# Optimization experiments

Measured on AMD Instinct MI355X. Metric: run time of the kernel, lower is better.

The kernel has to match this reference:

```python
import jax, jax.numpy as jnp
import numpy as np

N = 100000   # nodes
E = 3200000  # edges
C = 256      # in_channels
H = 64       # hidden_channels
G = 512      # graphs in batch
FC = [128, 64, 32, 16]
OUT = 2
EPS = 1e-5


def _linear(key, fan_in, fan_out):
    k1, k2 = jax.random.split(key)
    s = 1.0 / np.sqrt(fan_in)
    W = jax.random.uniform(k1, (fan_in, fan_out), jnp.float32, -s, s)
    b = jax.random.uniform(k2, (fan_out,), jnp.float32, -s, s)
    return W, b


def setup_inputs() -> dict:
    key = jax.random.key(0)
    ks = jax.random.split(key, 12)
    x = jax.random.normal(ks[0], (N, C), jnp.float32)
    edge_index = jax.random.randint(ks[1], (2, E), 0, N, dtype=jnp.int64)
    batch = jnp.sort(jax.random.randint(ks[2], (N,), 0, G, dtype=jnp.int64))
    w1, b1 = _linear(ks[3], C, H)
    w2, b2 = _linear(ks[4], H, H)
    g1 = jnp.ones((H,), jnp.float32); be1 = jnp.zeros((H,), jnp.float32)
    g2 = jnp.ones((H,), jnp.float32); be2 = jnp.zeros((H,), jnp.float32)
    fw1, fb1 = _linear(ks[5], H, FC[0])
    fw2, fb2 = _linear(ks[6], FC[0], FC[1])
    fw3, fb3 = _linear(ks[7], FC[1], FC[2])
    fw4, fb4 = _linear(ks[8], FC[2], FC[3])
    ow, ob = _linear(ks[9], FC[3], OUT)
    return dict(x=x, edge_index=edge_index, batch=batch,
                w1=w1, b1=b1, w2=w2, b2=b2,
                g1=g1, be1=be1, g2=g2, be2=be2,
                fw1=fw1, fb1=fb1, fw2=fw2, fb2=fb2,
                fw3=fw3, fb3=fb3, fw4=fw4, fb4=fb4,
                ow=ow, ob=ob)


def _gcn_layers(x, edge_index, w1, b1, w2, b2, g1, be1, g2, be2):
    # PyG GCNConv: add self loops, symmetric deg^-1/2 normalization, scatter-add at dst
    loops = jnp.arange(N, dtype=edge_index.dtype)
    src = jnp.concatenate([edge_index[0], loops])
    dst = jnp.concatenate([edge_index[1], loops])
    deg = jax.ops.segment_sum(jnp.ones((E + N,), jnp.float32), dst, num_segments=N)
    dis = jnp.where(deg > 0, jax.lax.rsqrt(jnp.maximum(deg, 1.0)), 0.0)
    norm = (dis[src] * dis[dst])[:, None]  # [E+N, 1]

    def conv(h, W, b):
        h = h @ W
        return jax.ops.segment_sum(h[src] * norm, dst, num_segments=N) + b

    def bn(h, g, be):  # BatchNorm1d over node dim (training-mode batch stats)
        m = jnp.mean(h, axis=0)
        v = jnp.var(h, axis=0)
        return (h - m) * jax.lax.rsqrt(v + EPS) * g + be

    h = bn(jax.nn.relu(conv(x, w1, b1)), g1, be1)   # dropout = identity (eval)
    h = bn(jax.nn.relu(conv(h, w2, b2)), g2, be2)
    return h


def reference(x, edge_index, batch, w1, b1, w2, b2, g1, be1, g2, be2,
              fw1, fb1, fw2, fb2, fw3, fb3, fw4, fb4, ow, ob):
    h = _gcn_layers(x, edge_index, w1, b1, w2, b2, g1, be1, g2, be2)
    # global_mean_pool over batch vector
    s = jax.ops.segment_sum(h, batch, num_segments=G)
    cnt = jax.ops.segment_sum(jnp.ones((N,), jnp.float32), batch, num_segments=G)
    p = s / jnp.maximum(cnt, 1.0)[:, None]  # [G, H]
    h = jax.nn.relu(p @ fw1 + fb1)
    h = jax.nn.relu(h @ fw2 + fb2)
    h = jax.nn.relu(h @ fw3 + fb3)
    h = jax.nn.relu(h @ fw4 + fb4)
    return h @ ow + ob  # [G, OUT]
```

## Files before the change

kernel.cpp:

```cpp
#include <hip/hip_runtime.h>
#include <hip/hip_fp16.h>

#define N_NODES 100000
#define E_EDGES 3200000
#define NG      512
#define BN_EPS  1e-5f

#define BSH     7
#define BNODES  128
#define NBUCK   782
#define NCHUNK  1024
#define CHUNK   3125

__global__ __launch_bounds__(256) void k_zero(float* __restrict__ stats1,
                                              float* __restrict__ stats2,
                                              float* __restrict__ sums,
                                              float* __restrict__ cnt) {
  int i = blockIdx.x * 256 + threadIdx.x;
  if (i < 128) { stats1[i] = 0.f; stats2[i] = 0.f; }
  if (i < NG * 64) sums[i] = 0.f;
  if (i < NG) cnt[i] = 0.f;
}

__global__ __launch_bounds__(256) void kb_hist(const int* __restrict__ ei,
                                               int* __restrict__ counts) {
  __shared__ int h[NBUCK];
  const int c = blockIdx.x, tid = threadIdx.x;
  for (int b = tid; b < NBUCK; b += 256) h[b] = 0;
  __syncthreads();
  const int* dst = ei + E_EDGES + c * CHUNK;
  for (int i = tid; i < CHUNK; i += 256) atomicAdd(&h[dst[i] >> BSH], 1);
  __syncthreads();
  for (int b = tid; b < NBUCK; b += 256) counts[b * NCHUNK + c] = h[b];
}

__global__ __launch_bounds__(1024) void kb_scan1(int* __restrict__ counts,
                                                 int* __restrict__ btot) {
  __shared__ int sm[NCHUNK];
  const int b = blockIdx.x, tid = threadIdx.x;
  const int cval = counts[b * NCHUNK + tid];
  int val = cval;
  sm[tid] = val;
  __syncthreads();
  for (int off = 1; off < NCHUNK; off <<= 1) {
    int t = (tid >= off) ? sm[tid - off] : 0;
    __syncthreads();
    val += t;
    sm[tid] = val;
    __syncthreads();
  }
  counts[b * NCHUNK + tid] = val - cval;
  if (tid == NCHUNK - 1) btot[b] = val;
}

__global__ __launch_bounds__(1024) void kb_scan2(const int* __restrict__ btot,
                                                 int* __restrict__ bbase) {
  __shared__ int sm[1024];
  const int tid = threadIdx.x;
  const int cval = (tid < NBUCK) ? btot[tid] : 0;
  int val = cval;
  sm[tid] = val;
  __syncthreads();
  for (int off = 1; off < 1024; off <<= 1) {
    int t = (tid >= off) ? sm[tid - off] : 0;
    __syncthreads();
    val += t;
    sm[tid] = val;
    __syncthreads();
  }
  if (tid < NBUCK) bbase[tid] = val - cval;
  if (tid == NBUCK - 1) bbase[NBUCK] = val;
}

__global__ __launch_bounds__(256) void kb_scatter(const int* __restrict__ ei,
                                                  const int* __restrict__ counts,
                                                  const int* __restrict__ bbase,
                                                  int* __restrict__ binned) {
  __shared__ int cur[NBUCK];
  const int c = blockIdx.x, tid = threadIdx.x;
  for (int b = tid; b < NBUCK; b += 256) cur[b] = bbase[b] + counts[b * NCHUNK + c];
  __syncthreads();
  const int* srcp = ei + c * CHUNK;
  const int* dstp = ei + E_EDGES + c * CHUNK;
  for (int i = tid; i < CHUNK; i += 256) {
    const int s = srcp[i], d = dstp[i];
    const int pos = atomicAdd(&cur[d >> BSH], 1);
    binned[pos] = ((d & (BNODES - 1)) << 17) | s;
  }
}

__global__ __launch_bounds__(256) void kb_degsort(const int* __restrict__ binned,
                                                  const int* __restrict__ bbase,
                                                  int* __restrict__ csr,
                                                  int* __restrict__ row_start,
                                                  float* __restrict__ dis) {
  __shared__ int h[BNODES];
  __shared__ int pre[BNODES];
  const int b = blockIdx.x, tid = threadIdx.x;
  if (tid < BNODES) h[tid] = 0;
  __syncthreads();
  const int e0 = bbase[b], e1 = bbase[b + 1];
  for (int i = e0 + tid; i < e1; i += 256) atomicAdd(&h[binned[i] >> 17], 1);
  __syncthreads();
  if (tid < BNODES) pre[tid] = h[tid];
  __syncthreads();
  for (int off = 1; off < BNODES; off <<= 1) {
    int t = (tid >= off && tid < BNODES) ? pre[tid - off] : 0;
    __syncthreads();
    if (tid < BNODES) pre[tid] += t;
    __syncthreads();
  }
  if (tid < BNODES) {
    const int n = b * BNODES + tid;
    const int ex = e0 + pre[tid] - h[tid];
    if (n < N_NODES) {
      row_start[n] = ex;
      dis[n] = rsqrtf((float)(h[tid] + 1));
    }
    h[tid] = ex;
  }
  if (b == NBUCK - 1 && tid == 0) row_start[N_NODES] = E_EDGES;
  __syncthreads();
  for (int i = e0 + tid; i < e1; i += 256) {
    const int v = binned[i];
    const int pos = atomicAdd(&h[v >> 17], 1);
    csr[pos] = v & 0x1FFFF;
  }
}

template <int K, bool BN>
__global__ __launch_bounds__(256) void k_gemm(const float* __restrict__ in,
                                              const float* __restrict__ W,
                                              const float* __restrict__ dis,
                                              const float* __restrict__ stats,
                                              const float* __restrict__ gam,
                                              const float* __restrict__ bet,
                                              __half* __restrict__ y) {
  __shared__ float xs[64 * 68];
  __shared__ float wsm[64 * 64];
  __shared__ float scv[64], shv[64];
  const int tid = threadIdx.x;
  const int n0 = blockIdx.x * 64;
  const int lane = tid & 63, wv = tid >> 6;
  const int nq = lane & 15;
  const int chb = wv * 16 + (lane >> 4) * 4;
  if (BN) {
    if (tid < 64) {
      const float m = stats[tid] * (1.0f / N_NODES);
      const float v = stats[64 + tid] * (1.0f / N_NODES) - m * m;
      const float sc = rsqrtf(v + BN_EPS) * gam[tid];
      scv[tid] = sc;
      shv[tid] = bet[tid] - m * sc;
    }
  }
  float a[4][4] = {{0,0,0,0},{0,0,0,0},{0,0,0,0},{0,0,0,0}};
  for (int c0 = 0; c0 < K; c0 += 64) {
    __syncthreads();
#pragma unroll
    for (int i = 0; i < 4; ++i) {
      const int idx = tid + i * 256;
      const int n = idx >> 4, c4 = (idx & 15) * 4;
      const int nn = min(n0 + n, N_NODES - 1);
      float4 v = *(const float4*)&in[(size_t)nn * K + c0 + c4];
      if (BN) {
        v.x = v.x * scv[c4] + shv[c4];
        v.y = v.y * scv[c4 + 1] + shv[c4 + 1];
        v.z = v.z * scv[c4 + 2] + shv[c4 + 2];
        v.w = v.w * scv[c4 + 3] + shv[c4 + 3];
      }
      *(float4*)&xs[n * 68 + c4] = v;
    }
#pragma unroll
    for (int i = 0; i < 4; ++i) {
      const int idx = tid + i * 256;
      const int c = idx >> 4, ch4 = (idx & 15) * 4;
      *(float4*)&wsm[c * 64 + ch4] = *(const float4*)&W[(size_t)(c0 + c) * 64 + ch4];
    }
    __syncthreads();
    for (int c = 0; c < 64; c += 4) {
      float wq[4][4];
#pragma unroll
      for (int cc = 0; cc < 4; ++cc) {
        const float4 w4 = *(const float4*)&wsm[(c + cc) * 64 + chb];
        wq[cc][0] = w4.x; wq[cc][1] = w4.y; wq[cc][2] = w4.z; wq[cc][3] = w4.w;
      }
#pragma unroll
      for (int i = 0; i < 4; ++i) {
        const float4 xv = *(const float4*)&xs[(nq + 16 * i) * 68 + c];
#pragma unroll
        for (int j = 0; j < 4; ++j) {
          a[i][j] = fmaf(xv.x, wq[0][j],
                    fmaf(xv.y, wq[1][j],
                    fmaf(xv.z, wq[2][j],
                    fmaf(xv.w, wq[3][j], a[i][j]))));
        }
      }
    }
  }
#pragma unroll
  for (int i = 0; i < 4; ++i) {
    const int n = n0 + nq + 16 * i;
    if (n < N_NODES) {
      const float d = dis[n];
      union { __half h[4]; float2 f; } u;
      u.h[0] = __float2half_rn(d * a[i][0]);
      u.h[1] = __float2half_rn(d * a[i][1]);
      u.h[2] = __float2half_rn(d * a[i][2]);
      u.h[3] = __float2half_rn(d * a[i][3]);
      *(float2*)&y[(size_t)n * 64 + chb] = u.f;
    }
  }
}

template <bool POOL>
__global__ __launch_bounds__(256) void k_gather(const int* __restrict__ csr,
                                                const int* __restrict__ rs,
                                                const __half* __restrict__ y,
                                                const float* __restrict__ dis,
                                                const float* __restrict__ bias,
                                                float* __restrict__ hout,
                                                float* __restrict__ stats,
                                                const int* __restrict__ batch,
                                                float* __restrict__ sums,
                                                float* __restrict__ cnt) {
  const int tid = threadIdx.x;
  const int lane = tid & 63;
  const int p = lane >> 3;
  const int c8 = lane & 7;
  const int ch = c8 * 8 + ((p & 1) << 2) + (p & 2) + ((p >> 2) & 1);
  const int wid = (blockIdx.x * 256 + tid) >> 6;
  const int nw = (gridDim.x * 256) >> 6;
  const int per = (N_NODES + nw - 1) / nw;
  const int n0 = wid * per;
  const int n1 = min(N_NODES, n0 + per);
  const float bch = bias[ch];
  float s1 = 0.f, s2 = 0.f;
  int curg = -1, run = 0;
  float px = 0.f;
  union U8 { float4 f4; __half2 h2[4]; };
  for (int n = n0; n < n1; ++n) {
    int e = rs[n];
    const int end = rs[n + 1];
    float acc[8] = {0.f, 0.f, 0.f, 0.f, 0.f, 0.f, 0.f, 0.f};
    if (p == 0) {
      U8 u;
      u.f4 = *(const float4*)&y[(size_t)n * 64 + c8 * 8];
#pragma unroll
      for (int k = 0; k < 4; ++k) {
        const float2 f = __half22float2(u.h2[k]);
        acc[2 * k] += f.x;
        acc[2 * k + 1] += f.y;
      }
    }
    while (e < end) {
      const int m = min(64, end - e);
      const int cidx = csr[(lane < m) ? e + lane : e];
      int o = 0;
      for (; o + 16 <= m; o += 16) {
        const int i0 = __shfl(cidx, o + p);
        const int i1 = __shfl(cidx, o + 8 + p);
        U8 u0, u1;
        u0.f4 = *(const float4*)&y[(size_t)i0 * 64 + c8 * 8];
        u1.f4 = *(const float4*)&y[(size_t)i1 * 64 + c8 * 8];
#pragma unroll
        for (int k = 0; k < 4; ++k) {
          const float2 f0 = __half22float2(u0.h2[k]);
          const float2 f1 = __half22float2(u1.h2[k]);
          acc[2 * k] += f0.x + f1.x;
          acc[2 * k + 1] += f0.y + f1.y;
        }
      }
      if (o + 8 <= m) {
        const int i0 = __shfl(cidx, o + p);
        U8 u0;
        u0.f4 = *(const float4*)&y[(size_t)i0 * 64 + c8 * 8];
#pragma unroll
        for (int k = 0; k < 4; ++k) {
          const float2 f0 = __half22float2(u0.h2[k]);
          acc[2 * k] += f0.x;
          acc[2 * k + 1] += f0.y;
        }
        o += 8;
      }
      if (o < m) {
        const int rem = m - o;
        const int i0 = __shfl(cidx, o + ((p < rem) ? p : 0));
        U8 u;
        u.f4 = *(const float4*)&y[(size_t)i0 * 64 + c8 * 8];
        if (p < rem) {
#pragma unroll
          for (int k = 0; k < 4; ++k) {
            const float2 f = __half22float2(u.h2[k]);
            acc[2 * k] += f.x;
            acc[2 * k + 1] += f.y;
          }
        }
      }
      e += m;
    }
    float t[4];
#pragma unroll
    for (int j = 0; j < 4; ++j) {
      const float send = (p & 1) ? acc[j] : acc[4 + j];
      const float keep = (p & 1) ? acc[4 + j] : acc[j];
      t[j] = keep + __shfl_xor(send, 8);
    }
    float u2v[2];
#pragma unroll
    for (int j = 0; j < 2; ++j) {
      const float send = (p & 2) ? t[j] : t[2 + j];
      const float keep = (p & 2) ? t[2 + j] : t[j];
      u2v[j] = keep + __shfl_xor(send, 16);
    }
    const float send3 = (p & 4) ? u2v[0] : u2v[1];
    const float keep3 = (p & 4) ? u2v[1] : u2v[0];
    const float s = keep3 + __shfl_xor(send3, 32);
    const float v = fmaxf(dis[n] * s + bch, 0.f);
    if (!POOL) hout[(size_t)n * 64 + ch] = v;
    s1 += v;
    s2 += v * v;
    if (POOL) {
      const int g = batch[n];
      if (g != curg) {
        if (run) {
          atomicAdd(&sums[curg * 64 + ch], px);
          if (lane == 0) atomicAdd(&cnt[curg], (float)run);
        }
        curg = g; run = 0; px = 0.f;
      }
      px += v;
      ++run;
    }
  }
  if (POOL && run) {
    atomicAdd(&sums[curg * 64 + ch], px);
    if (lane == 0) atomicAdd(&cnt[curg], (float)run);
  }
  __shared__ float r1[256], r2[256];
  const int wv = tid >> 6;
  r1[wv * 64 + ch] = s1;
  r2[wv * 64 + ch] = s2;
  __syncthreads();
  if (tid < 64) {
    atomicAdd(&stats[tid], r1[tid] + r1[tid + 64] + r1[tid + 128] + r1[tid + 192]);
  } else if (tid < 128) {
    const int h = tid - 64;
    atomicAdd(&stats[64 + h], r2[h] + r2[h + 64] + r2[h + 128] + r2[h + 192]);
  }
}

__global__ __launch_bounds__(128) void k_mlp(const float* __restrict__ sums,
                                             const float* __restrict__ cnt,
                                             const float* __restrict__ stats,
                                             const float* __restrict__ gam,
                                             const float* __restrict__ bet,
                                             const float* __restrict__ fw1, const float* __restrict__ fb1,
                                             const float* __restrict__ fw2, const float* __restrict__ fb2,
                                             const float* __restrict__ fw3, const float* __restrict__ fb3,
                                             const float* __restrict__ fw4, const float* __restrict__ fb4,
                                             const float* __restrict__ ow, const float* __restrict__ ob,
                                             float* __restrict__ out) {
  __shared__ float u0[128], u1[128];
  const int g = blockIdx.x, t = threadIdx.x;
  if (t < 64) {
    const float m = stats[t] * (1.0f / N_NODES);
    const float v = stats[64 + t] * (1.0f / N_NODES) - m * m;
    const float sc = rsqrtf(v + BN_EPS) * gam[t];
    const float sh = bet[t] - m * sc;
    u0[t] = (sums[g * 64 + t] / fmaxf(cnt[g], 1.0f)) * sc + sh;
  }
  __syncthreads();
  if (t < 128) {
    float a = fb1[t];
    for (int k = 0; k < 64; ++k) a = fmaf(u0[k], fw1[k * 128 + t], a);
    u1[t] = fmaxf(a, 0.f);
  }
  __syncthreads();
  if (t < 64) {
    float a = fb2[t];
    for (int k = 0; k < 128; ++k) a = fmaf(u1[k], fw2[k * 64 + t], a);
    u0[t] = fmaxf(a, 0.f);
  }
  __syncthreads();
  if (t < 32) {
    float a = fb3[t];
    for (int k = 0; k < 64; ++k) a = fmaf(u0[k], fw3[k * 32 + t], a);
    u1[t] = fmaxf(a, 0.f);
  }
  __syncthreads();
  if (t < 16) {
    float a = fb4[t];
    for (int k = 0; k < 32; ++k) a = fmaf(u1[k], fw4[k * 16 + t], a);
    u0[t] = fmaxf(a, 0.f);
  }
  __syncthreads();
  if (t < 2) {
    float a = ob[t];
    for (int k = 0; k < 16; ++k) a = fmaf(u0[k], ow[k * 2 + t], a);
    out[g * 2 + t] = a;
  }
}

extern "C" void kernel_launch(void* const* d_in, const int* in_sizes, int n_in,
                              void* d_out, int out_size, void* d_ws, size_t ws_size,
                              hipStream_t stream) {
  const float* x    = (const float*)d_in[0];
  const int*   ei   = (const int*)d_in[1];
  const int*   batch= (const int*)d_in[2];
  const float* w1   = (const float*)d_in[3];
  const float* b1   = (const float*)d_in[4];
  const float* w2   = (const float*)d_in[5];
  const float* b2   = (const float*)d_in[6];
  const float* g1   = (const float*)d_in[7];
  const float* be1  = (const float*)d_in[8];
  const float* g2   = (const float*)d_in[9];
  const float* be2  = (const float*)d_in[10];
  const float* fw1  = (const float*)d_in[11]; const float* fb1 = (const float*)d_in[12];
  const float* fw2  = (const float*)d_in[13]; const float* fb2 = (const float*)d_in[14];
  const float* fw3  = (const float*)d_in[15]; const float* fb3 = (const float*)d_in[16];
  const float* fw4  = (const float*)d_in[17]; const float* fb4 = (const float*)d_in[18];
  const float* ow   = (const float*)d_in[19]; const float* ob  = (const float*)d_in[20];
  float* out = (float*)d_out;

  char* ws = (char*)d_ws;
  auto alloc = [&](size_t bytes) {
    void* p = ws;
    ws += (bytes + 255) & ~(size_t)255;
    return p;
  };
  float*  dis      = (float*)alloc((size_t)N_NODES * 4);
  int*    counts   = (int*)  alloc((size_t)NBUCK * NCHUNK * 4);
  int*    btot     = (int*)  alloc((size_t)NBUCK * 4);
  int*    bbase    = (int*)  alloc((size_t)(NBUCK + 1) * 4);
  int*    binned   = (int*)  alloc((size_t)E_EDGES * 4);
  int*    csr      = (int*)  alloc((size_t)E_EDGES * 4);
  int*    row_start= (int*)  alloc((size_t)(N_NODES + 1) * 4);
  __half* yH       = (__half*)alloc((size_t)N_NODES * 64 * 2);
  float*  hB       = (float*)alloc((size_t)N_NODES * 64 * 4);
  float*  stats1   = (float*)alloc(512);
  float*  stats2   = (float*)alloc(512);
  float*  sums     = (float*)alloc((size_t)NG * 64 * 4);
  float*  cnt      = (float*)alloc((size_t)NG * 4);

  const int nblkG = (N_NODES + 63) / 64;

  k_zero    <<<128, 256, 0, stream>>>(stats1, stats2, sums, cnt);
  kb_hist   <<<NCHUNK, 256, 0, stream>>>(ei, counts);
  kb_scan1  <<<NBUCK, NCHUNK, 0, stream>>>(counts, btot);
  kb_scan2  <<<1, 1024, 0, stream>>>(btot, bbase);
  kb_scatter<<<NCHUNK, 256, 0, stream>>>(ei, counts, bbase, binned);
  kb_degsort<<<NBUCK, 256, 0, stream>>>(binned, bbase, csr, row_start, dis);

  k_gemm<256, false><<<nblkG, 256, 0, stream>>>(x, w1, dis, nullptr, nullptr, nullptr, yH);
  k_gather<false><<<2048, 256, 0, stream>>>(csr, row_start, yH, dis, b1, hB, stats1,
                                            nullptr, nullptr, nullptr);

  k_gemm<64, true><<<nblkG, 256, 0, stream>>>(hB, w2, dis, stats1, g1, be1, yH);
  k_gather<true><<<2048, 256, 0, stream>>>(csr, row_start, yH, dis, b2, nullptr, stats2,
                                           batch, sums, cnt);

  k_mlp<<<NG, 128, 0, stream>>>(sums, cnt, stats2, g2, be2,
                                fw1, fb1, fw2, fb2, fw3, fb3, fw4, fb4, ow, ob, out);
}
```

Measured before the change: 564.1 us.

## Use split-fp16 MFMA for the first-layer GEMM

Replaces the FP32 SIMT GEMM for x@W1 with a matrix-core kernel. Each operand is split into high and low fp16 parts and three MFMA 16x16x32 products are accumulated to keep near-fp32 accuracy. A small pre-kernel transposes and splits W1. This aims to cut the compute cost of the 100000x256x64 GEMM, at the price of extra conversion work and some precision loss from dropping the low-by-low term.

```diff
diff --git a/kernel.cpp b/kernel.cpp
--- a/kernel.cpp
+++ b/kernel.cpp
@@ -11,6 +11,9 @@
 #define NBUCK   782
 #define NCHUNK  1024
 #define CHUNK   3125
+
+typedef _Float16 f16x8 __attribute__((ext_vector_type(8)));
+typedef float    f32x4 __attribute__((ext_vector_type(4)));
 
 __global__ __launch_bounds__(256) void k_zero(float* __restrict__ stats1,
                                               float* __restrict__ stats2,
@@ -125,6 +128,89 @@
     const int v = binned[i];
     const int pos = atomicAdd(&h[v >> 17], 1);
     csr[pos] = v & 0x1FFFF;
+  }
+}
+
+__global__ __launch_bounds__(256) void k_wsplit(const float* __restrict__ W,
+                                                __half* __restrict__ wth,
+                                                __half* __restrict__ wtl) {
+  const int i = blockIdx.x * 256 + threadIdx.x;
+  if (i < 64 * 256) {
+    const int ch = i >> 8, k = i & 255;
+    const float v = W[k * 64 + ch];
+    const __half hi = __float2half_rn(v);
+    wth[i] = hi;
+    wtl[i] = __float2half_rn(v - __half2float(hi));
+  }
+}
+
+__global__ __launch_bounds__(256) void k_gemm1(const float* __restrict__ x,
+                                               const __half* __restrict__ wth,
+                                               const __half* __restrict__ wtl,
+                                               const float* __restrict__ dis,
+                                               __half* __restrict__ y) {
+  __shared__ __half xh[64][72], xl[64][72];
+  __shared__ __half wh[64][72], wl[64][72];
+  const int tid = threadIdx.x;
+  const int n0 = blockIdx.x * 64;
+  const int w = tid >> 6, lane = tid & 63;
+  const int l15 = lane & 15;
+  const int kb = (lane >> 4) << 3;
+  const int row4 = (lane >> 4) << 2;
+  f32x4 acc[4] = {{0.f,0.f,0.f,0.f},{0.f,0.f,0.f,0.f},
+                  {0.f,0.f,0.f,0.f},{0.f,0.f,0.f,0.f}};
+  for (int k0 = 0; k0 < 256; k0 += 64) {
+    __syncthreads();
+#pragma unroll
+    for (int i = 0; i < 4; ++i) {
+      const int idx = tid + i * 256;
+      const int n = idx >> 4, c4 = (idx & 15) * 4;
+      const int nn = min(n0 + n, N_NODES - 1);
+      const float4 v = *(const float4*)&x[(size_t)nn * 256 + k0 + c4];
+      const __half h0 = __float2half_rn(v.x), h1 = __float2half_rn(v.y),
+                   h2 = __float2half_rn(v.z), h3 = __float2half_rn(v.w);
+      union { __half h[4]; float2 f; } uh = {{h0, h1, h2, h3}};
+      *(float2*)&xh[n][c4] = uh.f;
+      union { __half h[4]; float2 f; } ul = {{
+          __float2half_rn(v.x - __half2float(h0)),
+          __float2half_rn(v.y - __half2float(h1)),
+          __float2half_rn(v.z - __half2float(h2)),
+          __float2half_rn(v.w - __half2float(h3))}};
+      *(float2*)&xl[n][c4] = ul.f;
+    }
+#pragma unroll
+    for (int i = 0; i < 2; ++i) {
+      const int idx = tid + i * 256;
+      const int ch = idx >> 3, k8 = (idx & 7) * 8;
+      *(float4*)&wh[ch][k8] = *(const float4*)&wth[ch * 256 + k0 + k8];
+      *(float4*)&wl[ch][k8] = *(const float4*)&wtl[ch * 256 + k0 + k8];
+    }
+    __syncthreads();
+#pragma unroll
+    for (int ks = 0; ks < 2; ++ks) {
+      const int kk = ks * 32 + kb;
+      const f16x8 ah = *(const f16x8*)&xh[w * 16 + l15][kk];
+      const f16x8 al = *(const f16x8*)&xl[w * 16 + l15][kk];
+#pragma unroll
+      for (int t = 0; t < 4; ++t) {
+        const f16x8 bh = *(const f16x8*)&wh[t * 16 + l15][kk];
+        const f16x8 bl = *(const f16x8*)&wl[t * 16 + l15][kk];
+        acc[t] = __builtin_amdgcn_mfma_f32_16x16x32_f16(ah, bh, acc[t], 0, 0, 0);
+        acc[t] = __builtin_amdgcn_mfma_f32_16x16x32_f16(ah, bl, acc[t], 0, 0, 0);
+        acc[t] = __builtin_amdgcn_mfma_f32_16x16x32_f16(al, bh, acc[t], 0, 0, 0);
+      }
+    }
+  }
+#pragma unroll
+  for (int j = 0; j < 4; ++j) {
+    const int n = n0 + w * 16 + row4 + j;
+    if (n < N_NODES) {
+      const float d = dis[n];
+#pragma unroll
+      for (int t = 0; t < 4; ++t) {
+        y[(size_t)n * 64 + t * 16 + l15] = __float2half_rn(d * acc[t][j]);
+      }
+    }
   }
 }
 
@@ -441,17 +527,20 @@
   float*  stats2   = (float*)alloc(512);
   float*  sums     = (float*)alloc((size_t)NG * 64 * 4);
   float*  cnt      = (float*)alloc((size_t)NG * 4);
+  __half* wth      = (__half*)alloc((size_t)64 * 256 * 2);
+  __half* wtl      = (__half*)alloc((size_t)64 * 256 * 2);
 
   const int nblkG = (N_NODES + 63) / 64;
 
   k_zero    <<<128, 256, 0, stream>>>(stats1, stats2, sums, cnt);
+  k_wsplit  <<<64, 256, 0, stream>>>(w1, wth, wtl);
   kb_hist   <<<NCHUNK, 256, 0, stream>>>(ei, counts);
   kb_scan1  <<<NBUCK, NCHUNK, 0, stream>>>(counts, btot);
   kb_scan2  <<<1, 1024, 0, stream>>>(btot, bbase);
   kb_scatter<<<NCHUNK, 256, 0, stream>>>(ei, counts, bbase, binned);
   kb_degsort<<<NBUCK, 256, 0, stream>>>(binned, bbase, csr, row_start, dis);
 
-  k_gemm<256, false><<<nblkG, 256, 0, stream>>>(x, w1, dis, nullptr, nullptr, nullptr, yH);
+  k_gemm1<<<nblkG, 256, 0, stream>>>(x, wth, wtl, dis, yH);
   k_gather<false><<<2048, 256, 0, stream>>>(csr, row_start, yH, dis, b1, hB, stats1,
                                             nullptr, nullptr, nullptr);
 
```

Measured after the change: 555.5 us. No clear change (-1.5%).
